# Kernel tuning notes

Measured on AMD Instinct MI355X. Metric: run time of the kernel, lower is better.

The kernel has to match this reference:

```python
import jax, jax.numpy as jnp
import numpy as np

N, E, G = 100000, 300000, 4096
ND, ED, H, ZI, ZS, NE, L = 64, 16, 256, 128, 128, 8, 3
LAMBDA_GRL = 1.0


def setup_inputs() -> dict:
    key = jax.random.key(0)
    ks = iter(jax.random.split(key, 64))
    def nrm(shape, scale=0.05):
        return jax.random.normal(next(ks), shape, jnp.float32) * scale
    inp = {
        'x': jax.random.normal(next(ks), (N, ND), jnp.float32),
        'edge_index': jax.random.randint(next(ks), (2, E), 0, N),
        'edge_attr': jax.random.normal(next(ks), (E, ED), jnp.float32),
        'batch': jnp.sort(jax.random.randint(next(ks), (N,), 0, G)),
        'node_W': nrm((ND, H)), 'node_b': nrm((H,)),
        'conv_eps': jnp.zeros((L,), jnp.float32),
        'edge_W': nrm((L, ED, H)), 'edge_b': nrm((L, H)),
        'mlp_W1': nrm((L, H, H)), 'mlp_b1': nrm((L, H)),
        'mlp_W2': nrm((L, H, H)), 'mlp_b2': nrm((L, H)),
        'gn_w': jnp.ones((L, H), jnp.float32), 'gn_b': jnp.zeros((L, H), jnp.float32),
        'gn_ms': jnp.ones((L, H), jnp.float32),
        'finv_W1': nrm((H, ZI)), 'finv_b1': nrm((ZI,)),
        'finv_W2': nrm((ZI, ZI)), 'finv_b2': nrm((ZI,)),
        'fspu_W1': nrm((H, ZS)), 'fspu_b1': nrm((ZS,)),
        'fspu_W2': nrm((ZS, ZS)), 'fspu_b2': nrm((ZS,)),
        'pred_W1': nrm((ZI, ZI)), 'pred_b1': nrm((ZI,)),
        'pred_W2': nrm((ZI, 1)), 'pred_b2': nrm((1,)),
        'adv_W1': nrm((ZI, ZI)), 'adv_b1': nrm((ZI,)),
        'adv_W2': nrm((ZI, NE)), 'adv_b2': nrm((NE,)),
    }
    return inp


def _mlp2(h, W1, b1, W2, b2):
    return jax.nn.relu(h @ W1 + b1) @ W2 + b2


def reference(x, edge_index, edge_attr, batch, node_W, node_b, conv_eps,
              edge_W, edge_b, mlp_W1, mlp_b1, mlp_W2, mlp_b2,
              gn_w, gn_b, gn_ms,
              finv_W1, finv_b1, finv_W2, finv_b2,
              fspu_W1, fspu_b1, fspu_W2, fspu_b2,
              pred_W1, pred_b1, pred_W2, pred_b2,
              adv_W1, adv_b1, adv_W2, adv_b2):
    src, dst = edge_index[0], edge_index[1]
    cnt = jax.ops.segment_sum(jnp.ones((N, 1), jnp.float32), batch, num_segments=G)
    cnt = jnp.maximum(cnt, 1.0)
    h = x @ node_W + node_b  # [N,H]
    for l in range(L):
        # GINEConv: sum_j relu(x_j + lin(e_ij))
        e = edge_attr @ edge_W[l] + edge_b[l]            # [E,H]
        m = jax.nn.relu(h[src] + e)                      # [E,H]
        agg = jax.ops.segment_sum(m, dst, num_segments=N)
        h = _mlp2((1.0 + conv_eps[l]) * h + agg, mlp_W1[l], mlp_b1[l], mlp_W2[l], mlp_b2[l])
        # GraphNorm
        mean = jax.ops.segment_sum(h, batch, num_segments=G) / cnt  # [G,H]
        out = h - gn_ms[l] * mean[batch]
        var = jax.ops.segment_sum(out * out, batch, num_segments=G) / cnt
        h = out * jax.lax.rsqrt(var[batch] + 1e-5) * gn_w[l] + gn_b[l]
        h = jax.nn.relu(h)  # dropout is identity at eval
    hg = jax.ops.segment_sum(h, batch, num_segments=G) / cnt  # global_mean_pool [G,H]
    z_inv = _mlp2(hg, finv_W1, finv_b1, finv_W2, finv_b2)
    z_spu = _mlp2(hg, fspu_W1, fspu_b1, fspu_W2, fspu_b2)
    yhat = _mlp2(z_inv, pred_W1, pred_b1, pred_W2, pred_b2)[:, 0]
    # gradient reversal: identity fwd, -lambda on bwd
    grl = jax.lax.stop_gradient(z_inv) * (1.0 + LAMBDA_GRL) - LAMBDA_GRL * z_inv
    envhat = _mlp2(grl, adv_W1, adv_b1, adv_W2, adv_b2)
    return (hg, z_inv, z_spu, yhat, envhat)
```

## Files before the change

### kernel.cpp

```cpp
#include <hip/hip_runtime.h>
#include <hip/hip_bf16.h>

typedef __bf16 bf16_t;
typedef __bf16 bf16x8 __attribute__((ext_vector_type(8)));
typedef __bf16 bf16x4 __attribute__((ext_vector_type(4)));
typedef float  f32x4  __attribute__((ext_vector_type(4)));

static constexpr int N_NODES = 100000;
static constexpr int N_EDGES = 300000;
static constexpr int N_GRAPH = 4096;
static constexpr int H  = 256;
static constexpr int ND = 64;
static constexpr int ZIC = 128;
static constexpr int NE = 8;
static constexpr int SCAN_B = 1024;

__device__ __forceinline__ int clampi(int v, int lo, int hi) {
  return v < lo ? lo : (v > hi ? hi : v);
}

__device__ __forceinline__ void dma16(const bf16_t* g, bf16_t* lds_base) {
  __builtin_amdgcn_global_load_lds(
      (const __attribute__((address_space(1))) void*)g,
      (__attribute__((address_space(3))) void*)lds_base, 16, 0, 0);
}

__global__ void compute_starts_kernel(const int* __restrict__ batch,
                                      int* __restrict__ starts, int N, int G) {
  int i = blockIdx.x * blockDim.x + threadIdx.x;
  if (i >= N) return;
  int b = clampi(batch[i], 0, G - 1);
  if (i == 0) {
    for (int g = 0; g <= b; ++g) starts[g] = 0;
  } else {
    int p = clampi(batch[i - 1], 0, G - 1);
    for (int g = p + 1; g <= b; ++g) starts[g] = i;
  }
  if (i == N - 1) {
    for (int g = b + 1; g <= G; ++g) starts[g] = N;
  }
}

__global__ void zero2_kernel(int* __restrict__ a, int* __restrict__ b, int N) {
  int i = blockIdx.x * blockDim.x + threadIdx.x;
  if (i < N) { a[i] = 0; b[i] = 0; }
}

__global__ void count_deg_kernel(const int* __restrict__ dst, int* __restrict__ counts, int E, int N) {
  int e = blockIdx.x * blockDim.x + threadIdx.x;
  if (e < E) atomicAdd(&counts[clampi(dst[e], 0, N - 1)], 1);
}

__global__ __launch_bounds__(SCAN_B) void scan1_kernel(const int* __restrict__ counts,
                                                       int* __restrict__ offs,
                                                       int* __restrict__ bsum, int N) {
  __shared__ int tmp[SCAN_B];
  int i = blockIdx.x * SCAN_B + threadIdx.x;
  int v = (i < N) ? counts[i] : 0;
  tmp[threadIdx.x] = v;
  __syncthreads();
  for (int d = 1; d < SCAN_B; d <<= 1) {
    int t = (threadIdx.x >= d) ? tmp[threadIdx.x - d] : 0;
    __syncthreads();
    tmp[threadIdx.x] += t;
    __syncthreads();
  }
  if (i < N) offs[i + 1] = tmp[threadIdx.x];
  if (threadIdx.x == SCAN_B - 1) bsum[blockIdx.x] = tmp[SCAN_B - 1];
  if (i == 0) offs[0] = 0;
}

__global__ void scan2_kernel(int* __restrict__ bsum, int nblk) {
  if (blockIdx.x == 0 && threadIdx.x == 0) {
    int run = 0;
    for (int b = 0; b < nblk; ++b) { int v = bsum[b]; bsum[b] = run; run += v; }
  }
}

__global__ __launch_bounds__(SCAN_B) void scan3_kernel(int* __restrict__ offs,
                                                       const int* __restrict__ bsum, int N) {
  int i = blockIdx.x * SCAN_B + threadIdx.x;
  if (i < N) offs[i + 1] += bsum[blockIdx.x];
}

__global__ void fill_scatter_kernel(const int* __restrict__ src, const int* __restrict__ dst,
                                    const float* __restrict__ eattr,
                                    const int* __restrict__ offs, int* __restrict__ cursor,
                                    int* __restrict__ src_srt, bf16_t* __restrict__ eat16,
                                    int E, int N) {
  int e = blockIdx.x * blockDim.x + threadIdx.x;
  if (e >= E) return;
  int d = clampi(dst[e], 0, N - 1);
  int pos = offs[d] + atomicAdd(&cursor[d], 1);
  if ((unsigned)pos >= (unsigned)E) return;
  int s = src[e];
  src_srt[pos] = ((unsigned)s < (unsigned)N_NODES) ? s : 0;
  const float* ea = eattr + (size_t)e * 16;
  union { bf16_t b[16]; uint4 u[2]; } pk;
#pragma unroll
  for (int k = 0; k < 16; ++k) pk.b[k] = (bf16_t)ea[k];
  uint4* dst16 = (uint4*)(eat16 + ((size_t)pos << 4));
  dst16[0] = pk.u[0];
  dst16[1] = pk.u[1];
}

__global__ void build_ewt16_kernel(const float* __restrict__ edge_W,
                                   bf16_t* __restrict__ ewt) {
  int idx = blockIdx.x * blockDim.x + threadIdx.x;
  if (idx >= 3 * 256 * 16) return;
  int l = idx / (256 * 16);
  int rem = idx - l * 256 * 16;
  int n = rem >> 4, k = rem & 15;
  ewt[idx] = (bf16_t)edge_W[(size_t)l * 16 * 256 + k * 256 + n];
}

__global__ void transpose_kernel(const float* __restrict__ W,
                                 bf16_t* __restrict__ Wt, int K, int Nc,
                                 size_t srcStride, size_t dstStride) {
  __shared__ float tile[32][33];
  const float* Wz = W + (size_t)blockIdx.z * srcStride;
  bf16_t* Wtz = Wt + (size_t)blockIdx.z * dstStride;
  int n0 = blockIdx.x * 32, k0 = blockIdx.y * 32;
  int tx = threadIdx.x, ty = threadIdx.y;
  for (int i = ty; i < 32; i += 8)
    tile[i][tx] = Wz[(size_t)(k0 + i) * Nc + n0 + tx];
  __syncthreads();
  for (int i = ty; i < 32; i += 8)
    Wtz[(size_t)(n0 + i) * K + k0 + tx] = (bf16_t)tile[tx][i];
}

__device__ __forceinline__ void load8_to_lds(const bf16_t* p, bool valid, uint4* dst) {
  uint4 v = make_uint4(0u, 0u, 0u, 0u);
  if (valid) v = *(const uint4*)p;
  *dst = v;
}
__device__ __forceinline__ void load8_to_lds(const float* p, bool valid, uint4* dst) {
  float4 f0 = make_float4(0.f, 0.f, 0.f, 0.f), f1 = f0;
  if (valid) { f0 = *(const float4*)p; f1 = *(const float4*)(p + 4); }
  union { bf16_t b[8]; uint4 u; } pk;
  pk.b[0] = (bf16_t)f0.x; pk.b[1] = (bf16_t)f0.y;
  pk.b[2] = (bf16_t)f0.z; pk.b[3] = (bf16_t)f0.w;
  pk.b[4] = (bf16_t)f1.x; pk.b[5] = (bf16_t)f1.y;
  pk.b[6] = (bf16_t)f1.z; pk.b[7] = (bf16_t)f1.w;
  *dst = pk.u;
}

template<int K, bool RELU, bool OUTF32, typename TIN>
__global__ __launch_bounds__(256) void gemm128_kernel(
    const TIN* __restrict__ U, const bf16_t* __restrict__ Wt,
    const float* __restrict__ bias, void* __restrict__ Out, int M, int Nc) {
  constexpr int LDT = 72;
  __shared__ bf16_t Ut[128 * LDT];
  __shared__ bf16_t Wl[128 * LDT];
  const int m0 = blockIdx.x * 128;
  const int n0 = blockIdx.y * 128;
  const int t = threadIdx.x;
  const int lane = t & 63;
  const int wave = t >> 6;
  const int wm = (wave >> 1) * 64;
  const int wn = (wave & 1) * 64;
  const int srow = t >> 1;
  const int sk = (t & 1) * 32;
  const int lr = lane & 15;
  const int lq = lane >> 4;
  const bool aok = (m0 + srow) < M;
  f32x4 acc[4][4] = {};

  for (int k0 = 0; k0 < K; k0 += 64) {
    const TIN* up = U + (size_t)(m0 + srow) * K + k0 + sk;
    const bf16_t* wp = Wt + (size_t)(n0 + srow) * K + k0 + sk;
#pragma unroll
    for (int q = 0; q < 4; ++q) {
      load8_to_lds(up + q * 8, aok, (uint4*)&Ut[srow * LDT + sk + q * 8]);
      load8_to_lds(wp + q * 8, true, (uint4*)&Wl[srow * LDT + sk + q * 8]);
    }
    __syncthreads();
#pragma unroll
    for (int s = 0; s < 2; ++s) {
      bf16x8 a[4], b[4];
#pragma unroll
      for (int mt = 0; mt < 4; ++mt)
        a[mt] = *(const bf16x8*)(&Ut[(wm + mt * 16 + lr) * LDT + s * 32 + lq * 8]);
#pragma unroll
      for (int nt = 0; nt < 4; ++nt)
        b[nt] = *(const bf16x8*)(&Wl[(wn + nt * 16 + lr) * LDT + s * 32 + lq * 8]);
#pragma unroll
      for (int mt = 0; mt < 4; ++mt)
#pragma unroll
        for (int nt = 0; nt < 4; ++nt)
          acc[mt][nt] = __builtin_amdgcn_mfma_f32_16x16x32_bf16(
              a[mt], b[nt], acc[mt][nt], 0, 0, 0);
    }
    __syncthreads();
  }

#pragma unroll
  for (int mt = 0; mt < 4; ++mt)
#pragma unroll
    for (int nt = 0; nt < 4; ++nt) {
      int col = n0 + wn + nt * 16 + lr;
      float bcol = bias[col];
#pragma unroll
      for (int r = 0; r < 4; ++r) {
        int row = m0 + wm + mt * 16 + lq * 4 + r;
        if (row < M) {
          float vv = acc[mt][nt][r] + bcol;
          if (RELU) vv = vv > 0.f ? vv : 0.f;
          if (OUTF32) ((float*)Out)[(size_t)row * Nc + col] = vv;
          else        ((bf16_t*)Out)[(size_t)row * Nc + col] = (bf16_t)vv;
        }
      }
    }
}

template<int K, bool RELU, bool OUTF32, typename TIN>
__global__ __launch_bounds__(256) void gemm64x2_kernel(
    const TIN* __restrict__ U0, const bf16_t* __restrict__ Wt0,
    const float* __restrict__ b0, void* __restrict__ O0,
    const TIN* __restrict__ U1, const bf16_t* __restrict__ Wt1,
    const float* __restrict__ b1, void* __restrict__ O1, int M, int Nc) {
  constexpr int LDT = 72;
  __shared__ bf16_t Ut[64 * LDT];
  __shared__ bf16_t Wl[64 * LDT];
  const TIN*    U    = blockIdx.z ? U1 : U0;
  const bf16_t* Wt   = blockIdx.z ? Wt1 : Wt0;
  const float*  bias = blockIdx.z ? b1 : b0;
  void*         Out  = blockIdx.z ? O1 : O0;
  const int m0 = blockIdx.x * 64;
  const int n0 = blockIdx.y * 64;
  const int t = threadIdx.x;
  const int lane = t & 63;
  const int wave = t >> 6;
  const int wm = (wave >> 1) * 32;
  const int wn = (wave & 1) * 32;
  const int srow = t >> 2;
  const int sk = (t & 3) * 8;
  const int lr = lane & 15;
  const int lq = lane >> 4;
  const bool aok = (m0 + srow) < M;
  f32x4 acc[2][2] = {};

  for (int k0 = 0; k0 < K; k0 += 64) {
    const TIN* up = U + (size_t)(m0 + srow) * K + k0 + sk;
    const bf16_t* wp = Wt + (size_t)(n0 + srow) * K + k0 + sk;
    load8_to_lds(up,      aok, (uint4*)&Ut[srow * LDT + sk]);
    load8_to_lds(up + 32, aok, (uint4*)&Ut[srow * LDT + sk + 32]);
    load8_to_lds(wp,      true, (uint4*)&Wl[srow * LDT + sk]);
    load8_to_lds(wp + 32, true, (uint4*)&Wl[srow * LDT + sk + 32]);
    __syncthreads();
#pragma unroll
    for (int s = 0; s < 2; ++s) {
      bf16x8 a[2], b[2];
#pragma unroll
      for (int mt = 0; mt < 2; ++mt)
        a[mt] = *(const bf16x8*)(&Ut[(wm + mt * 16 + lr) * LDT + s * 32 + lq * 8]);
#pragma unroll
      for (int nt = 0; nt < 2; ++nt)
        b[nt] = *(const bf16x8*)(&Wl[(wn + nt * 16 + lr) * LDT + s * 32 + lq * 8]);
#pragma unroll
      for (int mt = 0; mt < 2; ++mt)
#pragma unroll
        for (int nt = 0; nt < 2; ++nt)
          acc[mt][nt] = __builtin_amdgcn_mfma_f32_16x16x32_bf16(
              a[mt], b[nt], acc[mt][nt], 0, 0, 0);
    }
    __syncthreads();
  }

#pragma unroll
  for (int mt = 0; mt < 2; ++mt)
#pragma unroll
    for (int nt = 0; nt < 2; ++nt) {
      int col = n0 + wn + nt * 16 + lr;
      float bcol = bias[col];
#pragma unroll
      for (int r = 0; r < 4; ++r) {
        int row = m0 + wm + mt * 16 + lq * 4 + r;
        if (row < M) {
          float vv = acc[mt][nt][r] + bcol;
          if (RELU) vv = vv > 0.f ? vv : 0.f;
          if (OUTF32) ((float*)Out)[(size_t)row * Nc + col] = vv;
          else        ((bf16_t*)Out)[(size_t)row * Nc + col] = (bf16_t)vv;
        }
      }
    }
}

template<int K, bool RELU, bool OUTF32>
__global__ __launch_bounds__(256) void gemm128_dma_kernel(
    const bf16_t* __restrict__ U, const bf16_t* __restrict__ Wt,
    const float* __restrict__ bias, void* __restrict__ Out, int M, int Nc) {
  __shared__ bf16_t Ut[128 * 64];
  __shared__ bf16_t Wl[128 * 64];
  const int t = threadIdx.x;
  const int lane = t & 63;
  const int wave = t >> 6;
  const int m0 = blockIdx.x * 128;
  const int n0 = blockIdx.y * 128;
  const int wm = (wave >> 1) * 64;
  const int wn = (wave & 1) * 64;
  const int lr = lane & 15;
  const int lq = lane >> 4;
  const int subrow = wave * 8 + (lane >> 3);
  const int lchunk = (lane & 7) ^ (lane >> 3);
  f32x4 acc[4][4] = {};

  for (int k0 = 0; k0 < K; k0 += 64) {
#pragma unroll
    for (int q = 0; q < 4; ++q) {
      const int row = q * 32 + subrow;
      int urow = m0 + row; if (urow >= M) urow = M - 1;
      dma16(U + (size_t)urow * K + k0 + lchunk * 8, &Ut[(q * 32 + wave * 8) * 64]);
      dma16(Wt + (size_t)(n0 + row) * K + k0 + lchunk * 8, &Wl[(q * 32 + wave * 8) * 64]);
    }
    __syncthreads();
#pragma unroll
    for (int s = 0; s < 2; ++s) {
      bf16x8 a[4], b[4];
#pragma unroll
      for (int mt = 0; mt < 4; ++mt)
        a[mt] = *(const bf16x8*)(&Ut[(wm + mt * 16 + lr) * 64 + (((s * 4 + lq) ^ (lr & 7)) << 3)]);
#pragma unroll
      for (int nt = 0; nt < 4; ++nt)
        b[nt] = *(const bf16x8*)(&Wl[(wn + nt * 16 + lr) * 64 + (((s * 4 + lq) ^ (lr & 7)) << 3)]);
#pragma unroll
      for (int mt = 0; mt < 4; ++mt)
#pragma unroll
        for (int nt = 0; nt < 4; ++nt)
          acc[mt][nt] = __builtin_amdgcn_mfma_f32_16x16x32_bf16(
              a[mt], b[nt], acc[mt][nt], 0, 0, 0);
    }
    __syncthreads();
  }

#pragma unroll
  for (int mt = 0; mt < 4; ++mt)
#pragma unroll
    for (int nt = 0; nt < 4; ++nt) {
      int col = n0 + wn + nt * 16 + lr;
      float bcol = bias[col];
#pragma unroll
      for (int r = 0; r < 4; ++r) {
        int row = m0 + wm + mt * 16 + lq * 4 + r;
        if (row < M) {
          float vv = acc[mt][nt][r] + bcol;
          if (RELU) vv = vv > 0.f ? vv : 0.f;
          if (OUTF32) ((float*)Out)[(size_t)row * Nc + col] = vv;
          else        ((bf16_t*)Out)[(size_t)row * Nc + col] = (bf16_t)vv;
        }
      }
    }
}

__global__ __launch_bounds__(256) void gine_gather_mfma_kernel(
    const bf16_t* __restrict__ h, const bf16_t* __restrict__ eat16,
    const int* __restrict__ src_sorted, const int* __restrict__ offs,
    const bf16_t* __restrict__ ewt, const float* __restrict__ eb,
    const float* __restrict__ eps_p, bf16_t* __restrict__ u) {
  constexpr int HP = H + 8;
  __shared__ bf16_t slin[2][16 * HP];
  const int t = threadIdx.x;
  const int wave = t >> 6;
  const int lane = t & 63;
  const int lr = lane & 15;
  const int lq = lane >> 4;
  const int lane4 = lane * 4;
  const int n0 = blockIdx.x * 4;
  const int nodeN = n0 + wave;

  bf16x4 hs = *(const bf16x4*)(h + (size_t)nodeN * H + lane4);

  bf16x8 bfrag[4];
#pragma unroll
  for (int nt = 0; nt < 4; ++nt) {
    bf16x8 bv = {};
    if (lq < 2)
      bv = *(const bf16x8*)(ewt + ((wave * 64 + nt * 16 + lr) << 4) + (lq << 3));
    bfrag[nt] = bv;
  }
  float ebv[4];
#pragma unroll
  for (int i = 0; i < 4; ++i) ebv[i] = eb[lane4 + i];

  int bs = offs[n0], be = offs[n0 + 4];
  bs = clampi(bs, 0, N_EDGES);
  be = clampi(be, bs, N_EDGES);
  int ns = offs[nodeN], ne = offs[nodeN + 1];
  ns = clampi(ns, bs, be);
  ne = clampi(ne, ns, be);

  float acc[4] = {0.f, 0.f, 0.f, 0.f};
  int parity = 0;

  for (int cb = bs; cb < be; cb += 16, parity ^= 1) {
    int arow = cb + lr;
    if (arow >= N_EDGES) arow = N_EDGES - 1;
    bf16x8 afrag = {};
    if (lq < 2)
      afrag = *(const bf16x8*)(eat16 + ((size_t)arow << 4) + (lq << 3));

    int j0 = ns > cb ? ns : cb;
    int j1 = ne < cb + 16 ? ne : cb + 16;
    int sidx[4];
    bf16x4 hv[4];
    if (j0 < j1) {
#pragma unroll
      for (int q = 0; q < 4; ++q) {
        int jj = j0 + q; if (jj > j1 - 1) jj = j1 - 1;
        sidx[q] = src_sorted[jj];
      }
    }

    f32x4 c[4];
#pragma unroll
    for (int nt = 0; nt < 4; ++nt) {
      f32x4 z = {};
      c[nt] = __builtin_amdgcn_mfma_f32_16x16x32_bf16(afrag, bfrag[nt], z, 0, 0, 0);
    }
#pragma unroll
    for (int nt = 0; nt < 4; ++nt)
#pragma unroll
      for (int r = 0; r < 4; ++r)
        slin[parity][(lq * 4 + r) * HP + wave * 64 + nt * 16 + lr] = (bf16_t)c[nt][r];

    if (j0 < j1) {
#pragma unroll
      for (int q = 0; q < 4; ++q)
        hv[q] = *(const bf16x4*)(h + (size_t)sidx[q] * H + lane4);
    }

    __syncthreads();

    for (int jb = j0; jb < j1; jb += 4) {
      if (jb != j0) {
#pragma unroll
        for (int q = 0; q < 4; ++q) {
          int jj = jb + q; if (jj > j1 - 1) jj = j1 - 1;
          sidx[q] = src_sorted[jj];
        }
#pragma unroll
        for (int q = 0; q < 4; ++q)
          hv[q] = *(const bf16x4*)(h + (size_t)sidx[q] * H + lane4);
      }
#pragma unroll
      for (int q = 0; q < 4; ++q) {
        if (jb + q < j1) {
          bf16x4 lv = *(const bf16x4*)(&slin[parity][(jb + q - cb) * HP + lane4]);
#pragma unroll
          for (int i = 0; i < 4; ++i)
            acc[i] += fmaxf((float)hv[q][i] + (float)lv[i] + ebv[i], 0.f);
        }
      }
    }
  }

  const float sc = 1.0f + eps_p[0];
  union { bf16x4 v; uint2 b; } o;
#pragma unroll
  for (int i = 0; i < 4; ++i) o.v[i] = (bf16_t)(sc * (float)hs[i] + acc[i]);
  *(uint2*)(u + (size_t)nodeN * H + lane4) = o.b;
}

__global__ __launch_bounds__(256) void graphnorm_kernel(
    const bf16_t* __restrict__ v, bf16_t* __restrict__ hout,
    const int* __restrict__ starts,
    const float* __restrict__ w, const float* __restrict__ b,
    const float* __restrict__ ms, float* __restrict__ hg) {
  constexpr int RS = 9;
  constexpr int PS = 13;
  __shared__ float red[4 * 64 * RS];
  __shared__ float prm[64 * PS];
  const int g = blockIdx.x;
  const int t = threadIdx.x;
  const int lane = t & 63;
  const int wave = t >> 6;
  const int c0 = lane * 4;
  int s = starts[g], e = starts[g + 1];
  s = clampi(s, 0, N_NODES);
  e = clampi(e, s, N_NODES);
  const float cnt = (float)((e - s) > 1 ? (e - s) : 1);

  float sx[4] = {0.f, 0.f, 0.f, 0.f}, sxx[4] = {0.f, 0.f, 0.f, 0.f};
  {
    int i = s + wave;
    for (; i + 4 < e; i += 8) {
      bf16x4 x0 = *(const bf16x4*)(v + (size_t)i * H + c0);
      bf16x4 x1 = *(const bf16x4*)(v + (size_t)(i + 4) * H + c0);
#pragma unroll
      for (int j = 0; j < 4; ++j) {
        float f0 = (float)x0[j], f1 = (float)x1[j];
        sx[j] += f0 + f1; sxx[j] += f0 * f0 + f1 * f1;
      }
    }
    if (i < e) {
      bf16x4 x0 = *(const bf16x4*)(v + (size_t)i * H + c0);
#pragma unroll
      for (int j = 0; j < 4; ++j) {
        float f0 = (float)x0[j];
        sx[j] += f0; sxx[j] += f0 * f0;
      }
    }
  }
  float* myred = &red[(wave * 64 + lane) * RS];
#pragma unroll
  for (int j = 0; j < 4; ++j) { myred[j] = sx[j]; myred[4 + j] = sxx[j]; }
  __syncthreads();

  if (wave == 0) {
#pragma unroll
    for (int j = 0; j < 4; ++j) {
      float fsx = red[lane * RS + j] + red[(64 + lane) * RS + j] +
                  red[(128 + lane) * RS + j] + red[(192 + lane) * RS + j];
      float fsxx = red[lane * RS + 4 + j] + red[(64 + lane) * RS + 4 + j] +
                   red[(128 + lane) * RS + 4 + j] + red[(192 + lane) * RS + 4 + j];
      float mean = fsx / cnt;
      float sub = ms[c0 + j] * mean;
      float var = fsxx / cnt - 2.f * sub * mean + sub * sub;
      var = fmaxf(var, 0.f);
      prm[lane * PS + j] = sub;
      prm[lane * PS + 4 + j] = rsqrtf(var + 1e-5f) * w[c0 + j];
      prm[lane * PS + 8 + j] = b[c0 + j];
    }
  }
  __syncthreads();
  float sub[4], inv[4], bb[4];
#pragma unroll
  for (int j = 0; j < 4; ++j) {
    sub[j] = prm[lane * PS + j];
    inv[j] = prm[lane * PS + 4 + j];
    bb[j] = prm[lane * PS + 8 + j];
  }

  float psum[4] = {0.f, 0.f, 0.f, 0.f};
  {
    int i = s + wave;
    for (; i + 4 < e; i += 8) {
      bf16x4 x0 = *(const bf16x4*)(v + (size_t)i * H + c0);
      bf16x4 x1 = *(const bf16x4*)(v + (size_t)(i + 4) * H + c0);
      union { bf16x4 o; uint2 u; } p0, p1;
#pragma unroll
      for (int j = 0; j < 4; ++j) {
        float o0 = ((float)x0[j] - sub[j]) * inv[j] + bb[j];
        float o1 = ((float)x1[j] - sub[j]) * inv[j] + bb[j];
        o0 = o0 > 0.f ? o0 : 0.f;
        o1 = o1 > 0.f ? o1 : 0.f;
        psum[j] += o0 + o1;
        p0.o[j] = (bf16_t)o0; p1.o[j] = (bf16_t)o1;
      }
      *(uint2*)(hout + (size_t)i * H + c0) = p0.u;
      *(uint2*)(hout + (size_t)(i + 4) * H + c0) = p1.u;
    }
    if (i < e) {
      bf16x4 x0 = *(const bf16x4*)(v + (size_t)i * H + c0);
      union { bf16x4 o; uint2 u; } p0;
#pragma unroll
      for (int j = 0; j < 4; ++j) {
        float o0 = ((float)x0[j] - sub[j]) * inv[j] + bb[j];
        o0 = o0 > 0.f ? o0 : 0.f;
        psum[j] += o0;
        p0.o[j] = (bf16_t)o0;
      }
      *(uint2*)(hout + (size_t)i * H + c0) = p0.u;
    }
  }

  if (hg) {
#pragma unroll
    for (int j = 0; j < 4; ++j) myred[j] = psum[j];
    __syncthreads();
    if (wave == 0) {
#pragma unroll
      for (int j = 0; j < 4; ++j) {
        float p = red[lane * RS + j] + red[(64 + lane) * RS + j] +
                  red[(128 + lane) * RS + j] + red[(192 + lane) * RS + j];
        hg[(size_t)g * H + c0 + j] = p / cnt;
      }
    }
  }
}

__global__ void head_out2_kernel(const bf16_t* __restrict__ In1, const float* __restrict__ W1,
                                 const float* __restrict__ b1, float* __restrict__ O1,
                                 const bf16_t* __restrict__ In2, const float* __restrict__ W2,
                                 const float* __restrict__ b2, float* __restrict__ O2,
                                 int M) {
  int idx = blockIdx.x * blockDim.x + threadIdx.x;
  if (idx < M) {
    float acc = b1[0];
    const bf16_t* in = In1 + (size_t)idx * ZIC;
    for (int k = 0; k < ZIC; ++k) acc += (float)in[k] * W1[k];
    O1[idx] = acc;
  } else {
    int j = idx - M;
    if (j >= M * NE) return;
    int r = j >> 3, n = j & 7;
    float acc = b2[n];
    const bf16_t* in = In2 + (size_t)r * ZIC;
    for (int k = 0; k < ZIC; ++k) acc += (float)in[k] * W2[(size_t)k * NE + n];
    O2[j] = acc;
  }
}

extern "C" void kernel_launch(void* const* d_in, const int* in_sizes, int n_in,
                              void* d_out, int out_size, void* d_ws, size_t ws_size,
                              hipStream_t stream) {
  (void)in_sizes; (void)n_in; (void)out_size; (void)ws_size;
  const float* x        = (const float*)d_in[0];
  const int*   eidx     = (const int*)d_in[1];
  const float* eattr    = (const float*)d_in[2];
  const int*   batch    = (const int*)d_in[3];
  const float* node_W   = (const float*)d_in[4];
  const float* node_b   = (const float*)d_in[5];
  const float* conv_eps = (const float*)d_in[6];
  const float* edge_W   = (const float*)d_in[7];
  const float* edge_b   = (const float*)d_in[8];
  const float* mlp_W1   = (const float*)d_in[9];
  const float* mlp_b1   = (const float*)d_in[10];
  const float* mlp_W2   = (const float*)d_in[11];
  const float* mlp_b2   = (const float*)d_in[12];
  const float* gn_w     = (const float*)d_in[13];
  const float* gn_b     = (const float*)d_in[14];
  const float* gn_ms    = (const float*)d_in[15];
  const float* finv_W1  = (const float*)d_in[16];
  const float* finv_b1  = (const float*)d_in[17];
  const float* finv_W2  = (const float*)d_in[18];
  const float* finv_b2  = (const float*)d_in[19];
  const float* fspu_W1  = (const float*)d_in[20];
  const float* fspu_b1  = (const float*)d_in[21];
  const float* fspu_W2  = (const float*)d_in[22];
  const float* fspu_b2  = (const float*)d_in[23];
  const float* pred_W1  = (const float*)d_in[24];
  const float* pred_b1  = (const float*)d_in[25];
  const float* pred_W2  = (const float*)d_in[26];
  const float* pred_b2  = (const float*)d_in[27];
  const float* adv_W1   = (const float*)d_in[28];
  const float* adv_b1   = (const float*)d_in[29];
  const float* adv_W2   = (const float*)d_in[30];
  const float* adv_b2   = (const float*)d_in[31];
  float* out = (float*)d_out;

  float* out_hg = out;
  float* out_zi = out + (size_t)N_GRAPH * H;
  float* out_zs = out_zi + (size_t)N_GRAPH * ZIC;
  float* out_yh = out_zs + (size_t)N_GRAPH * ZIC;
  float* out_ev = out_yh + N_GRAPH;

  char* wp = (char*)d_ws;
  auto alloc = [&](size_t bytes) { char* p = wp; wp += (bytes + 255) & ~(size_t)255; return p; };
  bf16_t* A        = (bf16_t*)alloc((size_t)N_NODES * H * 2);
  bf16_t* B        = (bf16_t*)alloc((size_t)N_NODES * H * 2);
  bf16_t* Wt       = (bf16_t*)alloc((size_t)(H * ND + 6 * H * H) * 2);
  bf16_t* WtH      = (bf16_t*)alloc((size_t)(2 * ZIC * H + 4 * ZIC * ZIC) * 2);
  bf16_t* ewt16    = (bf16_t*)alloc((size_t)3 * 256 * 16 * 2);
  bf16_t* eat16    = (bf16_t*)alloc((size_t)N_EDGES * 16 * 2);
  int*    starts   = (int*)alloc((size_t)(N_GRAPH + 1) * 4);
  int*    counts   = (int*)alloc((size_t)N_NODES * 4);
  int*    cursor   = (int*)alloc((size_t)N_NODES * 4);
  int*    offs     = (int*)alloc((size_t)(N_NODES + 1) * 4);
  int*    bsum     = (int*)alloc((size_t)SCAN_B * 4);
  int*    src_srt  = (int*)alloc((size_t)N_EDGES * 4);
  bf16_t* tmp1     = (bf16_t*)alloc((size_t)N_GRAPH * ZIC * 2);
  bf16_t* tmp2     = (bf16_t*)alloc((size_t)N_GRAPH * ZIC * 2);

  const int* srcp = eidx;
  const int* dstp = eidx + N_EDGES;
  const int nscan = (N_NODES + SCAN_B - 1) / SCAN_B;

  compute_starts_kernel<<<(N_NODES + 255) / 256, 256, 0, stream>>>(batch, starts, N_NODES, N_GRAPH);

  zero2_kernel<<<(N_NODES + 255) / 256, 256, 0, stream>>>(counts, cursor, N_NODES);
  count_deg_kernel<<<(N_EDGES + 255) / 256, 256, 0, stream>>>(dstp, counts, N_EDGES, N_NODES);
  scan1_kernel<<<nscan, SCAN_B, 0, stream>>>(counts, offs, bsum, N_NODES);
  scan2_kernel<<<1, 64, 0, stream>>>(bsum, nscan);
  scan3_kernel<<<nscan, SCAN_B, 0, stream>>>(offs, bsum, N_NODES);
  fill_scatter_kernel<<<(N_EDGES + 255) / 256, 256, 0, stream>>>(
      srcp, dstp, eattr, offs, cursor, src_srt, eat16, N_EDGES, N_NODES);
  build_ewt16_kernel<<<(3 * 256 * 16 + 255) / 256, 256, 0, stream>>>(edge_W, ewt16);

  bf16_t* WtN = Wt;
  bf16_t* Wt1base = Wt + H * ND;
  bf16_t* Wt2base = Wt + H * ND + (size_t)H * H;
  auto Wt1l = [&](int l) { return Wt1base + (size_t)(2 * l) * H * H; };
  auto Wt2l = [&](int l) { return Wt2base + (size_t)(2 * l) * H * H; };
  transpose_kernel<<<dim3(H / 32, ND / 32, 1), dim3(32, 8), 0, stream>>>(node_W, WtN, ND, H, 0, 0);
  transpose_kernel<<<dim3(H / 32, H / 32, 3), dim3(32, 8), 0, stream>>>(
      mlp_W1, Wt1base, H, H, (size_t)H * H, (size_t)2 * H * H);
  transpose_kernel<<<dim3(H / 32, H / 32, 3), dim3(32, 8), 0, stream>>>(
      mlp_W2, Wt2base, H, H, (size_t)H * H, (size_t)2 * H * H);

  bf16_t* fT1 = WtH;
  bf16_t* fT2 = fT1 + ZIC * H;
  bf16_t* sT1 = fT2 + ZIC * ZIC;
  bf16_t* sT2 = sT1 + ZIC * H;
  bf16_t* pT1 = sT2 + ZIC * ZIC;
  bf16_t* aT1 = pT1 + ZIC * ZIC;
  transpose_kernel<<<dim3(ZIC / 32, H / 32, 1), dim3(32, 8), 0, stream>>>(finv_W1, fT1, H, ZIC, 0, 0);
  transpose_kernel<<<dim3(ZIC / 32, ZIC / 32, 1), dim3(32, 8), 0, stream>>>(finv_W2, fT2, ZIC, ZIC, 0, 0);
  transpose_kernel<<<dim3(ZIC / 32, H / 32, 1), dim3(32, 8), 0, stream>>>(fspu_W1, sT1, H, ZIC, 0, 0);
  transpose_kernel<<<dim3(ZIC / 32, ZIC / 32, 1), dim3(32, 8), 0, stream>>>(fspu_W2, sT2, ZIC, ZIC, 0, 0);
  transpose_kernel<<<dim3(ZIC / 32, ZIC / 32, 1), dim3(32, 8), 0, stream>>>(pred_W1, pT1, ZIC, ZIC, 0, 0);
  transpose_kernel<<<dim3(ZIC / 32, ZIC / 32, 1), dim3(32, 8), 0, stream>>>(adv_W1, aT1, ZIC, ZIC, 0, 0);

  dim3 ggrid((N_NODES + 127) / 128, H / 128);
  gemm128_kernel<ND, false, false><<<ggrid, 256, 0, stream>>>(x, WtN, node_b, A, N_NODES, H);

  for (int l = 0; l < 3; ++l) {
    gine_gather_mfma_kernel<<<N_NODES / 4, 256, 0, stream>>>(
        A, eat16, src_srt, offs, ewt16 + (size_t)l * 256 * 16,
        edge_b + l * H, conv_eps + l, B);
    gemm128_dma_kernel<H, true,  false><<<ggrid, 256, 0, stream>>>(B, Wt1l(l), mlp_b1 + l * H, A, N_NODES, H);
    gemm128_dma_kernel<H, false, false><<<ggrid, 256, 0, stream>>>(A, Wt2l(l), mlp_b2 + l * H, B, N_NODES, H);
    graphnorm_kernel<<<N_GRAPH, 256, 0, stream>>>(B, A, starts, gn_w + l * H, gn_b + l * H,
                                                  gn_ms + l * H, (l == 2) ? out_hg : nullptr);
  }

  dim3 hgrid2(N_GRAPH / 64, ZIC / 64, 2);
  gemm64x2_kernel<H, true, false, float><<<hgrid2, 256, 0, stream>>>(
      out_hg, fT1, finv_b1, tmp1, out_hg, sT1, fspu_b1, tmp2, N_GRAPH, ZIC);
  gemm64x2_kernel<ZIC, false, true, bf16_t><<<hgrid2, 256, 0, stream>>>(
      tmp1, fT2, finv_b2, out_zi, tmp2, sT2, fspu_b2, out_zs, N_GRAPH, ZIC);
  gemm64x2_kernel<ZIC, true, false, float><<<hgrid2, 256, 0, stream>>>(
      out_zi, pT1, pred_b1, tmp1, out_zi, aT1, adv_b1, tmp2, N_GRAPH, ZIC);
  head_out2_kernel<<<(N_GRAPH * (1 + NE) + 255) / 256, 256, 0, stream>>>(
      tmp1, pred_W2, pred_b2, out_yh, tmp2, adv_W2, adv_b2, out_ev, N_GRAPH);
}
```

Measured before the change: 747.6 us.

## Process 16 nodes per gather block and fuse counter zeroing into starts kernel

The GINE gather kernel now handles 16 destination nodes per block, with each wave owning 4 nodes instead of 1. This cuts the block count by 4x, and each block's edge-embedding MFMA tile is shared across more nodes, so redundant per-block setup and B-fragment loads are amortized. The zero-initialization of the degree counters is folded into compute_starts_kernel, removing one launch. The trade-offs are a larger per-wave register footprint (four accumulators and four hs vectors) and possible load imbalance across waves inside a block.

```diff
diff --git a/kernel.cpp b/kernel.cpp
--- a/kernel.cpp
+++ b/kernel.cpp
@@ -26,9 +26,13 @@
 }
 
 __global__ void compute_starts_kernel(const int* __restrict__ batch,
-                                      int* __restrict__ starts, int N, int G) {
+                                      int* __restrict__ starts,
+                                      int* __restrict__ counts,
+                                      int* __restrict__ cursor, int N, int G) {
   int i = blockIdx.x * blockDim.x + threadIdx.x;
   if (i >= N) return;
+  counts[i] = 0;
+  cursor[i] = 0;
   int b = clampi(batch[i], 0, G - 1);
   if (i == 0) {
     for (int g = 0; g <= b; ++g) starts[g] = 0;
@@ -39,11 +43,6 @@
   if (i == N - 1) {
     for (int g = b + 1; g <= G; ++g) starts[g] = N;
   }
-}
-
-__global__ void zero2_kernel(int* __restrict__ a, int* __restrict__ b, int N) {
-  int i = blockIdx.x * blockDim.x + threadIdx.x;
-  if (i < N) { a[i] = 0; b[i] = 0; }
 }
 
 __global__ void count_deg_kernel(const int* __restrict__ dst, int* __restrict__ counts, int E, int N) {
@@ -365,10 +364,13 @@
   const int lr = lane & 15;
   const int lq = lane >> 4;
   const int lane4 = lane * 4;
-  const int n0 = blockIdx.x * 4;
-  const int nodeN = n0 + wave;
-
-  bf16x4 hs = *(const bf16x4*)(h + (size_t)nodeN * H + lane4);
+  const int n0 = blockIdx.x * 16;
+  const int nodeB = n0 + wave * 4;
+
+  bf16x4 hs[4];
+#pragma unroll
+  for (int k = 0; k < 4; ++k)
+    hs[k] = *(const bf16x4*)(h + (size_t)(nodeB + k) * H + lane4);
 
   bf16x8 bfrag[4];
 #pragma unroll
@@ -382,14 +384,17 @@
 #pragma unroll
   for (int i = 0; i < 4; ++i) ebv[i] = eb[lane4 + i];
 
-  int bs = offs[n0], be = offs[n0 + 4];
+  int bs = offs[n0], be = offs[n0 + 16];
   bs = clampi(bs, 0, N_EDGES);
   be = clampi(be, bs, N_EDGES);
-  int ns = offs[nodeN], ne = offs[nodeN + 1];
-  ns = clampi(ns, bs, be);
-  ne = clampi(ne, ns, be);
-
-  float acc[4] = {0.f, 0.f, 0.f, 0.f};
+  int nb[5];
+#pragma unroll
+  for (int q = 0; q < 5; ++q) nb[q] = offs[nodeB + q];
+  nb[0] = clampi(nb[0], bs, be);
+#pragma unroll
+  for (int q = 1; q < 5; ++q) nb[q] = clampi(nb[q], nb[q - 1], be);
+
+  f32x4 accv[4] = {};
   int parity = 0;
 
   for (int cb = bs; cb < be; cb += 16, parity ^= 1) {
@@ -399,14 +404,14 @@
     if (lq < 2)
       afrag = *(const bf16x8*)(eat16 + ((size_t)arow << 4) + (lq << 3));
 
-    int j0 = ns > cb ? ns : cb;
-    int j1 = ne < cb + 16 ? ne : cb + 16;
+    int j0p = nb[0] > cb ? nb[0] : cb;
+    int j1p = nb[1] < cb + 16 ? nb[1] : cb + 16;
     int sidx[4];
     bf16x4 hv[4];
-    if (j0 < j1) {
+    if (j0p < j1p) {
 #pragma unroll
       for (int q = 0; q < 4; ++q) {
-        int jj = j0 + q; if (jj > j1 - 1) jj = j1 - 1;
+        int jj = j0p + q; if (jj > j1p - 1) jj = j1p - 1;
         sidx[q] = src_sorted[jj];
       }
     }
@@ -423,7 +428,7 @@
       for (int r = 0; r < 4; ++r)
         slin[parity][(lq * 4 + r) * HP + wave * 64 + nt * 16 + lr] = (bf16_t)c[nt][r];
 
-    if (j0 < j1) {
+    if (j0p < j1p) {
 #pragma unroll
       for (int q = 0; q < 4; ++q)
         hv[q] = *(const bf16x4*)(h + (size_t)sidx[q] * H + lane4);
@@ -431,34 +436,42 @@
 
     __syncthreads();
 
-    for (int jb = j0; jb < j1; jb += 4) {
-      if (jb != j0) {
+#pragma unroll
+    for (int k = 0; k < 4; ++k) {
+      int j0 = nb[k] > cb ? nb[k] : cb;
+      int j1 = nb[k + 1] < cb + 16 ? nb[k + 1] : cb + 16;
+      for (int jb = j0; jb < j1; jb += 4) {
+        if (k != 0 || jb != j0p) {
+#pragma unroll
+          for (int q = 0; q < 4; ++q) {
+            int jj = jb + q; if (jj > j1 - 1) jj = j1 - 1;
+            sidx[q] = src_sorted[jj];
+          }
+#pragma unroll
+          for (int q = 0; q < 4; ++q)
+            hv[q] = *(const bf16x4*)(h + (size_t)sidx[q] * H + lane4);
+        }
 #pragma unroll
         for (int q = 0; q < 4; ++q) {
-          int jj = jb + q; if (jj > j1 - 1) jj = j1 - 1;
-          sidx[q] = src_sorted[jj];
+          if (jb + q < j1) {
+            bf16x4 lv = *(const bf16x4*)(&slin[parity][(jb + q - cb) * HP + lane4]);
+#pragma unroll
+            for (int i = 0; i < 4; ++i)
+              accv[k][i] += fmaxf((float)hv[q][i] + (float)lv[i] + ebv[i], 0.f);
+          }
         }
-#pragma unroll
-        for (int q = 0; q < 4; ++q)
-          hv[q] = *(const bf16x4*)(h + (size_t)sidx[q] * H + lane4);
-      }
-#pragma unroll
-      for (int q = 0; q < 4; ++q) {
-        if (jb + q < j1) {
-          bf16x4 lv = *(const bf16x4*)(&slin[parity][(jb + q - cb) * HP + lane4]);
-#pragma unroll
-          for (int i = 0; i < 4; ++i)
-            acc[i] += fmaxf((float)hv[q][i] + (float)lv[i] + ebv[i], 0.f);
-        }
       }
     }
   }
 
   const float sc = 1.0f + eps_p[0];
-  union { bf16x4 v; uint2 b; } o;
-#pragma unroll
-  for (int i = 0; i < 4; ++i) o.v[i] = (bf16_t)(sc * (float)hs[i] + acc[i]);
-  *(uint2*)(u + (size_t)nodeN * H + lane4) = o.b;
+#pragma unroll
+  for (int k = 0; k < 4; ++k) {
+    union { bf16x4 v; uint2 b; } o;
+#pragma unroll
+    for (int i = 0; i < 4; ++i) o.v[i] = (bf16_t)(sc * (float)hs[k][i] + accv[k][i]);
+    *(uint2*)(u + (size_t)(nodeB + k) * H + lane4) = o.b;
+  }
 }
 
 __global__ __launch_bounds__(256) void graphnorm_kernel(
@@ -666,9 +679,8 @@
   const int* dstp = eidx + N_EDGES;
   const int nscan = (N_NODES + SCAN_B - 1) / SCAN_B;
 
-  compute_starts_kernel<<<(N_NODES + 255) / 256, 256, 0, stream>>>(batch, starts, N_NODES, N_GRAPH);
-
-  zero2_kernel<<<(N_NODES + 255) / 256, 256, 0, stream>>>(counts, cursor, N_NODES);
+  compute_starts_kernel<<<(N_NODES + 255) / 256, 256, 0, stream>>>(
+      batch, starts, counts, cursor, N_NODES, N_GRAPH);
   count_deg_kernel<<<(N_EDGES + 255) / 256, 256, 0, stream>>>(dstp, counts, N_EDGES, N_NODES);
   scan1_kernel<<<nscan, SCAN_B, 0, stream>>>(counts, offs, bsum, N_NODES);
   scan2_kernel<<<1, 64, 0, stream>>>(bsum, nscan);
@@ -705,7 +717,7 @@
   gemm128_kernel<ND, false, false><<<ggrid, 256, 0, stream>>>(x, WtN, node_b, A, N_NODES, H);
 
   for (int l = 0; l < 3; ++l) {
-    gine_gather_mfma_kernel<<<N_NODES / 4, 256, 0, stream>>>(
+    gine_gather_mfma_kernel<<<N_NODES / 16, 256, 0, stream>>>(
         A, eat16, src_srt, offs, ewt16 + (size_t)l * 256 * 16,
         edge_b + l * H, conv_eps + l, B);
     gemm128_dma_kernel<H, true,  false><<<ggrid, 256, 0, stream>>>(B, Wt1l(l), mlp_b1 + l * H, A, N_NODES, H);
```

New measurement: 836.8 us. 1.12x slower.

## Widen MLP GEMM tile to full 256 columns and fold zeroing into starts kernel

Applied to the files above, without the earlier changes.

The per-layer MLP GEMMs now use 512-thread blocks covering a 128x256 output tile. Each A row-block is loaded once instead of twice across two column blocks, which halves activation reads from global memory. The separate zeroing kernel is merged into compute_starts_kernel to save one launch. In exchange, LDS use per block grows and there are half as many blocks, which may lower occupancy.

```diff
diff --git a/kernel.cpp b/kernel.cpp
--- a/kernel.cpp
+++ b/kernel.cpp
@@ -26,9 +26,13 @@
 }
 
 __global__ void compute_starts_kernel(const int* __restrict__ batch,
-                                      int* __restrict__ starts, int N, int G) {
+                                      int* __restrict__ starts,
+                                      int* __restrict__ counts,
+                                      int* __restrict__ cursor, int N, int G) {
   int i = blockIdx.x * blockDim.x + threadIdx.x;
   if (i >= N) return;
+  counts[i] = 0;
+  cursor[i] = 0;
   int b = clampi(batch[i], 0, G - 1);
   if (i == 0) {
     for (int g = 0; g <= b; ++g) starts[g] = 0;
@@ -39,11 +43,6 @@
   if (i == N - 1) {
     for (int g = b + 1; g <= G; ++g) starts[g] = N;
   }
-}
-
-__global__ void zero2_kernel(int* __restrict__ a, int* __restrict__ b, int N) {
-  int i = blockIdx.x * blockDim.x + threadIdx.x;
-  if (i < N) { a[i] = 0; b[i] = 0; }
 }
 
 __global__ void count_deg_kernel(const int* __restrict__ dst, int* __restrict__ counts, int E, int N) {
@@ -286,32 +285,35 @@
     }
 }
 
-template<int K, bool RELU, bool OUTF32>
-__global__ __launch_bounds__(256) void gemm128_dma_kernel(
+template<int K, bool RELU>
+__global__ __launch_bounds__(512) void gemm256_dma_kernel(
     const bf16_t* __restrict__ U, const bf16_t* __restrict__ Wt,
-    const float* __restrict__ bias, void* __restrict__ Out, int M, int Nc) {
+    const float* __restrict__ bias, bf16_t* __restrict__ Out, int M) {
   __shared__ bf16_t Ut[128 * 64];
-  __shared__ bf16_t Wl[128 * 64];
+  __shared__ bf16_t Wl[256 * 64];
   const int t = threadIdx.x;
   const int lane = t & 63;
   const int wave = t >> 6;
   const int m0 = blockIdx.x * 128;
-  const int n0 = blockIdx.y * 128;
-  const int wm = (wave >> 1) * 64;
-  const int wn = (wave & 1) * 64;
+  const int wm = (wave >> 2) * 64;
+  const int wn = (wave & 3) * 64;
   const int lr = lane & 15;
   const int lq = lane >> 4;
-  const int subrow = wave * 8 + (lane >> 3);
-  const int lchunk = (lane & 7) ^ (lane >> 3);
+  const int subrow = lane >> 3;
+  const int lchunk = (lane & 7) ^ subrow;
   f32x4 acc[4][4] = {};
 
   for (int k0 = 0; k0 < K; k0 += 64) {
 #pragma unroll
-    for (int q = 0; q < 4; ++q) {
-      const int row = q * 32 + subrow;
-      int urow = m0 + row; if (urow >= M) urow = M - 1;
-      dma16(U + (size_t)urow * K + k0 + lchunk * 8, &Ut[(q * 32 + wave * 8) * 64]);
-      dma16(Wt + (size_t)(n0 + row) * K + k0 + lchunk * 8, &Wl[(q * 32 + wave * 8) * 64]);
+    for (int c = 0; c < 2; ++c) {
+      int urow = m0 + c * 64 + wave * 8 + subrow;
+      if (urow >= M) urow = M - 1;
+      dma16(U + (size_t)urow * K + k0 + lchunk * 8, &Ut[(c * 64 + wave * 8) * 64]);
+    }
+#pragma unroll
+    for (int c = 0; c < 4; ++c) {
+      int wrow = c * 64 + wave * 8 + subrow;
+      dma16(Wt + (size_t)wrow * K + k0 + lchunk * 8, &Wl[(c * 64 + wave * 8) * 64]);
     }
     __syncthreads();
 #pragma unroll
@@ -337,7 +339,7 @@
   for (int mt = 0; mt < 4; ++mt)
 #pragma unroll
     for (int nt = 0; nt < 4; ++nt) {
-      int col = n0 + wn + nt * 16 + lr;
+      int col = wn + nt * 16 + lr;
       float bcol = bias[col];
 #pragma unroll
       for (int r = 0; r < 4; ++r) {
@@ -345,8 +347,7 @@
         if (row < M) {
           float vv = acc[mt][nt][r] + bcol;
           if (RELU) vv = vv > 0.f ? vv : 0.f;
-          if (OUTF32) ((float*)Out)[(size_t)row * Nc + col] = vv;
-          else        ((bf16_t*)Out)[(size_t)row * Nc + col] = (bf16_t)vv;
+          Out[(size_t)row * H + col] = (bf16_t)vv;
         }
       }
     }
@@ -666,9 +667,8 @@
   const int* dstp = eidx + N_EDGES;
   const int nscan = (N_NODES + SCAN_B - 1) / SCAN_B;
 
-  compute_starts_kernel<<<(N_NODES + 255) / 256, 256, 0, stream>>>(batch, starts, N_NODES, N_GRAPH);
-
-  zero2_kernel<<<(N_NODES + 255) / 256, 256, 0, stream>>>(counts, cursor, N_NODES);
+  compute_starts_kernel<<<(N_NODES + 255) / 256, 256, 0, stream>>>(
+      batch, starts, counts, cursor, N_NODES, N_GRAPH);
   count_deg_kernel<<<(N_EDGES + 255) / 256, 256, 0, stream>>>(dstp, counts, N_EDGES, N_NODES);
   scan1_kernel<<<nscan, SCAN_B, 0, stream>>>(counts, offs, bsum, N_NODES);
   scan2_kernel<<<1, 64, 0, stream>>>(bsum, nscan);
@@ -704,12 +704,13 @@
   dim3 ggrid((N_NODES + 127) / 128, H / 128);
   gemm128_kernel<ND, false, false><<<ggrid, 256, 0, stream>>>(x, WtN, node_b, A, N_NODES, H);
 
+  const int mblocks = (N_NODES + 127) / 128;
   for (int l = 0; l < 3; ++l) {
     gine_gather_mfma_kernel<<<N_NODES / 4, 256, 0, stream>>>(
         A, eat16, src_srt, offs, ewt16 + (size_t)l * 256 * 16,
         edge_b + l * H, conv_eps + l, B);
-    gemm128_dma_kernel<H, true,  false><<<ggrid, 256, 0, stream>>>(B, Wt1l(l), mlp_b1 + l * H, A, N_NODES, H);
-    gemm128_dma_kernel<H, false, false><<<ggrid, 256, 0, stream>>>(A, Wt2l(l), mlp_b2 + l * H, B, N_NODES, H);
+    gemm256_dma_kernel<H, true ><<<mblocks, 512, 0, stream>>>(B, Wt1l(l), mlp_b1 + l * H, A, N_NODES);
+    gemm256_dma_kernel<H, false><<<mblocks, 512, 0, stream>>>(A, Wt2l(l), mlp_b2 + l * H, B, N_NODES);
     graphnorm_kernel<<<N_GRAPH, 256, 0, stream>>>(B, A, starts, gn_w + l * H, gn_b + l * H,
                                                   gn_ms + l * H, (l == 2) ? out_hg : nullptr);
   }
```

Result: faster. 729.0 us (-2.5%).
